# Performance work log

Measured on AMD Instinct MI355X. Metric: run time of the kernel, lower is better.

Reference implementation:

```python
import jax, jax.numpy as jnp
import numpy as np

B, N = 128, 2048
QUERY_DIM, NODE_DIM, OUT_DIM = 256, 128, 256
LAMBDA_INIT = 0.8
LN_EPS = 1e-5


def setup_inputs() -> dict:
    key = jax.random.key(0)
    ks = jax.random.split(key, 8)
    fp_vec = jax.random.normal(ks[0], (B, QUERY_DIM), dtype=jnp.float32)
    node_mat = jax.random.normal(ks[1], (B, N, NODE_DIM), dtype=jnp.float32)
    mask = jax.random.uniform(ks[2], (B, N)) < 0.75
    s = 1.0 / np.sqrt(QUERY_DIM)
    Wq1 = jax.random.uniform(ks[3], (NODE_DIM, QUERY_DIM), minval=-s, maxval=s, dtype=jnp.float32)
    Wq2 = jax.random.uniform(ks[4], (NODE_DIM, QUERY_DIM), minval=-s, maxval=s, dtype=jnp.float32)
    s2 = 1.0 / np.sqrt(NODE_DIM)
    Wk = jax.random.uniform(ks[5], (NODE_DIM, NODE_DIM), minval=-s2, maxval=s2, dtype=jnp.float32)
    Wv = jax.random.uniform(ks[6], (OUT_DIM, NODE_DIM), minval=-s2, maxval=s2, dtype=jnp.float32)
    lambda_logit = jnp.zeros((1,), dtype=jnp.float32)
    gamma = jnp.ones((OUT_DIM,), dtype=jnp.float32)
    beta = jnp.zeros((OUT_DIM,), dtype=jnp.float32)
    return {"fp_vec": fp_vec, "node_mat": node_mat, "mask": mask,
            "Wq1": Wq1, "Wq2": Wq2, "Wk": Wk, "Wv": Wv,
            "lambda_logit": lambda_logit, "gamma": gamma, "beta": beta}


def reference(fp_vec, node_mat, mask, Wq1, Wq2, Wk, Wv, lambda_logit, gamma, beta):
    node_dim = node_mat.shape[-1]
    inv_scale = 1.0 / jnp.sqrt(jnp.asarray(node_dim, jnp.float32))
    # projections (torch Linear: y = x @ W.T)
    q1 = fp_vec @ Wq1.T            # (B, node_dim)
    q2 = fp_vec @ Wq2.T            # (B, node_dim)
    k = jnp.einsum('bnd,ed->bne', node_mat, Wk)   # (B, N, node_dim)
    v = jnp.einsum('bnd,od->bno', node_mat, Wv)   # (B, N, out_dim)
    # single-query scores over nodes
    s1 = jnp.einsum('bd,bnd->bn', q1, k) * inv_scale
    s2 = jnp.einsum('bd,bnd->bn', q2, k) * inv_scale
    pad = jnp.where(mask, 0.0, -1e9).astype(s1.dtype)  # (B, N)
    A1 = jax.nn.softmax(s1 + pad, axis=-1)
    A2 = jax.nn.softmax(s2 + pad, axis=-1)
    lam = LAMBDA_INIT + jax.nn.sigmoid(lambda_logit) * 0.2  # (1,)
    A_diff = A1 - lam * A2         # dropout inactive (eval)
    z = jnp.einsum('bn,bno->bo', A_diff, v)  # (B, out_dim)
    # LayerNorm
    mu = jnp.mean(z, axis=-1, keepdims=True)
    var = jnp.mean(jnp.square(z - mu), axis=-1, keepdims=True)
    return (z - mu) * jax.lax.rsqrt(var + LN_EPS) * gamma + beta
```

## Files before the change

### kernel.cpp

```cpp
#include <hip/hip_runtime.h>
#include <hip/hip_bf16.h>
#include <math.h>

#define BB 128
#define NN 2048
#define ND 128
#define QD 256
#define OD 256
#define CHUNKS 16
#define ROWS_PER_CHUNK (NN / CHUNKS)
#define PART_STRIDE 260

#define EXP2F(x) __builtin_amdgcn_exp2f(x)

__global__ __launch_bounds__(128) void proj_kernel(
    const float* __restrict__ fp_vec, const float* __restrict__ Wq1,
    const float* __restrict__ Wq2, const float* __restrict__ Wk,
    float* __restrict__ qk1g, float* __restrict__ qk2g)
{
  __shared__ __align__(16) float fp_s[QD];
  __shared__ float q1_s[ND];
  __shared__ float q2_s[ND];
  const int b = blockIdx.x, t = threadIdx.x;
  fp_s[t]       = fp_vec[b * QD + t];
  fp_s[t + 128] = fp_vec[b * QD + 128 + t];
  __syncthreads();
  float a1 = 0.f, a2 = 0.f;
  const float4* w1p = (const float4*)(Wq1 + t * QD);
  const float4* w2p = (const float4*)(Wq2 + t * QD);
  #pragma unroll 8
  for (int q = 0; q < QD / 4; ++q) {
    float4 wa = w1p[q], wb = w2p[q];
    float4 f = *(const float4*)&fp_s[q * 4];
    a1 += f.x * wa.x + f.y * wa.y + f.z * wa.z + f.w * wa.w;
    a2 += f.x * wb.x + f.y * wb.y + f.z * wb.z + f.w * wb.w;
  }
  q1_s[t] = a1;
  q2_s[t] = a2;
  __syncthreads();
  float k1 = 0.f, k2 = 0.f;
  #pragma unroll 8
  for (int e = 0; e < ND; ++e) {
    float wv = Wk[e * ND + t];
    k1 += q1_s[e] * wv;
    k2 += q2_s[e] * wv;
  }
  const float cscale = 0.08838834764831845f * 1.4426950408889634f;
  qk1g[b * ND + t] = k1 * cscale;
  qk2g[b * ND + t] = k2 * cscale;
}

__global__ __launch_bounds__(256) void attn_kernel(
    const float* __restrict__ node, const int* __restrict__ mask,
    const float* __restrict__ qk1g, const float* __restrict__ qk2g,
    float* __restrict__ part)
{
  const int bid = blockIdx.x;
  const int b = bid >> 4;
  const int c = bid & (CHUNKS - 1);
  const int t = threadIdx.x;
  const int wave = t >> 6;
  const int lane = t & 63;
  const int half = lane >> 5;
  const int hl = lane & 31;

  __shared__ float pad_s[ROWS_PER_CHUNK];
  __shared__ float sl1[8], sl2[8];
  __shared__ __align__(16) float sw1[8][ND];
  __shared__ __align__(16) float sw2[8][ND];

  const int chunk_row0 = c * ROWS_PER_CHUNK;
  if (t < ROWS_PER_CHUNK)
    pad_s[t] = mask[b * NN + chunk_row0 + t] ? 0.f : -1e9f;
  __syncthreads();

  const float4 qk1 = *(const float4*)(qk1g + b * ND + hl * 4);
  const float4 qk2 = *(const float4*)(qk2g + b * ND + hl * 4);

  const int row_base = chunk_row0 + wave * 32;
  const float* nb = node + (size_t)b * NN * ND;

  float l1 = 0.f, l2 = 0.f;
  float4 w1 = make_float4(0.f, 0.f, 0.f, 0.f);
  float4 w2 = make_float4(0.f, 0.f, 0.f, 0.f);

  #pragma unroll 8
  for (int j = 0; j < 16; ++j) {
    const int rw = 2 * j + half;
    const float4 x = *(const float4*)(nb + (size_t)(row_base + rw) * ND + hl * 4);
    const float pad = pad_s[wave * 32 + rw];

    float d1 = x.x * qk1.x + x.y * qk1.y + x.z * qk1.z + x.w * qk1.w;
    float d2 = x.x * qk2.x + x.y * qk2.y + x.z * qk2.z + x.w * qk2.w;
    #pragma unroll
    for (int off = 1; off < 32; off <<= 1) {
      d1 += __shfl_xor(d1, off, 64);
      d2 += __shfl_xor(d2, off, 64);
    }
    const float p1 = EXP2F(d1 + pad);
    const float p2 = EXP2F(d2 + pad);
    l1 += p1;
    l2 += p2;
    w1.x += p1 * x.x; w1.y += p1 * x.y; w1.z += p1 * x.z; w1.w += p1 * x.w;
    w2.x += p2 * x.x; w2.y += p2 * x.y; w2.z += p2 * x.z; w2.w += p2 * x.w;
  }

  const int hidx = wave * 2 + half;
  if (hl == 0) { sl1[hidx] = l1; sl2[hidx] = l2; }
  *(float4*)&sw1[hidx][hl * 4] = w1;
  *(float4*)&sw2[hidx][hl * 4] = w2;
  __syncthreads();

  float* po = part + (size_t)bid * PART_STRIDE;
  if (t == 0) {
    float L1 = 0.f, L2 = 0.f;
    #pragma unroll
    for (int i = 0; i < 8; ++i) { L1 += sl1[i]; L2 += sl2[i]; }
    po[0] = L1; po[1] = L2;
  }
  if (t < ND) {
    float W1 = 0.f, W2 = 0.f;
    #pragma unroll
    for (int i = 0; i < 8; ++i) {
      W1 += sw1[i][t];
      W2 += sw2[i][t];
    }
    po[4 + t]   = W1;
    po[132 + t] = W2;
  }
}

__global__ __launch_bounds__(256) void finish_kernel(
    const float* __restrict__ part, const float* __restrict__ Wv,
    const float* __restrict__ lambda_logit, const float* __restrict__ gamma,
    const float* __restrict__ beta, float* __restrict__ out)
{
  const int b = blockIdx.x, t = threadIdx.x;
  __shared__ __align__(16) float wd_s[ND];
  __shared__ float red[8];

  const float lam = 0.8f + 0.2f / (1.f + __expf(-lambda_logit[0]));
  const float* pb = part + (size_t)b * CHUNKS * PART_STRIDE;

  if (t < ND) {
    float L1 = 0.f, L2 = 0.f, W1 = 0.f, W2 = 0.f;
    #pragma unroll
    for (int i = 0; i < CHUNKS; ++i) {
      const float* pc = pb + (size_t)i * PART_STRIDE;
      L1 += pc[0];
      L2 += pc[1];
      W1 += pc[4 + t];
      W2 += pc[132 + t];
    }
    wd_s[t] = W1 / L1 - lam * (W2 / L2);
  }
  __syncthreads();

  float z = 0.f;
  const float4* wvp = (const float4*)(Wv + t * ND);
  #pragma unroll 8
  for (int d = 0; d < ND / 4; ++d) {
    const float4 w = wvp[d];
    const float4 f = *(const float4*)&wd_s[d * 4];
    z += f.x * w.x + f.y * w.y + f.z * w.z + f.w * w.w;
  }

  const int wave = t >> 6, lane = t & 63;
  float s = z;
  #pragma unroll
  for (int off = 32; off; off >>= 1) s += __shfl_xor(s, off, 64);
  if (lane == 0) red[wave] = s;
  __syncthreads();
  const float mu = (red[0] + red[1] + red[2] + red[3]) * (1.f / OD);
  const float dz = z - mu;
  float vs = dz * dz;
  #pragma unroll
  for (int off = 32; off; off >>= 1) vs += __shfl_xor(vs, off, 64);
  if (lane == 0) red[wave + 4] = vs;
  __syncthreads();
  const float var = (red[4] + red[5] + red[6] + red[7]) * (1.f / OD);
  out[b * OD + t] = dz * rsqrtf(var + 1e-5f) * gamma[t] + beta[t];
}

extern "C" void kernel_launch(void* const* d_in, const int* in_sizes, int n_in,
                              void* d_out, int out_size, void* d_ws, size_t ws_size,
                              hipStream_t stream) {
  const float* fp_vec = (const float*)d_in[0];
  const float* node   = (const float*)d_in[1];
  const int*   mask   = (const int*)d_in[2];
  const float* Wq1    = (const float*)d_in[3];
  const float* Wq2    = (const float*)d_in[4];
  const float* Wk     = (const float*)d_in[5];
  const float* Wv     = (const float*)d_in[6];
  const float* ll     = (const float*)d_in[7];
  const float* gamma  = (const float*)d_in[8];
  const float* beta   = (const float*)d_in[9];
  float* out = (float*)d_out;

  float* qk1g = (float*)d_ws;
  float* qk2g = qk1g + BB * ND;
  float* part = qk2g + BB * ND;

  proj_kernel<<<BB, 128, 0, stream>>>(fp_vec, Wq1, Wq2, Wk, qk1g, qk2g);
  attn_kernel<<<BB * CHUNKS, 256, 0, stream>>>(node, mask, qk1g, qk2g, part);
  finish_kernel<<<BB, 256, 0, stream>>>(part, Wv, ll, gamma, beta, out);
}
```

Measured before the change: 239.6 us.

## Double-buffer node tiles through LDS with register prefetch in attention kernel

```diff
diff --git a/kernel.cpp b/kernel.cpp
--- a/kernel.cpp
+++ b/kernel.cpp
@@ -9,6 +9,8 @@
 #define OD 256
 #define CHUNKS 16
 #define ROWS_PER_CHUNK (NN / CHUNKS)
+#define TILE_ROWS 16
+#define TILES (ROWS_PER_CHUNK / TILE_ROWS)
 #define PART_STRIDE 260
 
 #define EXP2F(x) __builtin_amdgcn_exp2f(x)
@@ -64,69 +66,94 @@
   const int half = lane >> 5;
   const int hl = lane & 31;
 
+  __shared__ __align__(16) float tile_s[2][TILE_ROWS * ND];
   __shared__ float pad_s[ROWS_PER_CHUNK];
-  __shared__ float sl1[8], sl2[8];
-  __shared__ __align__(16) float sw1[8][ND];
-  __shared__ __align__(16) float sw2[8][ND];
+  __shared__ float sl1[4], sl2[4];
+  __shared__ __align__(16) float sw1[4][ND], sw2[4][ND];
 
   const int chunk_row0 = c * ROWS_PER_CHUNK;
   if (t < ROWS_PER_CHUNK)
     pad_s[t] = mask[b * NN + chunk_row0 + t] ? 0.f : -1e9f;
-  __syncthreads();
 
   const float4 qk1 = *(const float4*)(qk1g + b * ND + hl * 4);
   const float4 qk2 = *(const float4*)(qk2g + b * ND + hl * 4);
 
-  const int row_base = chunk_row0 + wave * 32;
-  const float* nb = node + (size_t)b * NN * ND;
+  const float4* gc = (const float4*)(node + (size_t)b * NN * ND
+                                     + (size_t)chunk_row0 * ND);
+
+  {
+    float4 a0 = gc[t];
+    float4 a1 = gc[t + 256];
+    float4* d = (float4*)tile_s[0];
+    d[t] = a0;
+    d[t + 256] = a1;
+  }
+  __syncthreads();
 
   float l1 = 0.f, l2 = 0.f;
   float4 w1 = make_float4(0.f, 0.f, 0.f, 0.f);
   float4 w2 = make_float4(0.f, 0.f, 0.f, 0.f);
 
-  #pragma unroll 8
-  for (int j = 0; j < 16; ++j) {
-    const int rw = 2 * j + half;
-    const float4 x = *(const float4*)(nb + (size_t)(row_base + rw) * ND + hl * 4);
-    const float pad = pad_s[wave * 32 + rw];
-
-    float d1 = x.x * qk1.x + x.y * qk1.y + x.z * qk1.z + x.w * qk1.w;
-    float d2 = x.x * qk2.x + x.y * qk2.y + x.z * qk2.z + x.w * qk2.w;
+  #pragma unroll
+  for (int tt = 0; tt < TILES; ++tt) {
+    float4 y0, y1;
+    if (tt + 1 < TILES) {
+      y0 = gc[(tt + 1) * (TILE_ROWS * ND / 4) + t];
+      y1 = gc[(tt + 1) * (TILE_ROWS * ND / 4) + t + 256];
+    }
+    __builtin_amdgcn_sched_barrier(0);
+
+    const float* buf = tile_s[tt & 1];
     #pragma unroll
-    for (int off = 1; off < 32; off <<= 1) {
-      d1 += __shfl_xor(d1, off, 64);
-      d2 += __shfl_xor(d2, off, 64);
-    }
-    const float p1 = EXP2F(d1 + pad);
-    const float p2 = EXP2F(d2 + pad);
-    l1 += p1;
-    l2 += p2;
-    w1.x += p1 * x.x; w1.y += p1 * x.y; w1.z += p1 * x.z; w1.w += p1 * x.w;
-    w2.x += p2 * x.x; w2.y += p2 * x.y; w2.z += p2 * x.z; w2.w += p2 * x.w;
-  }
-
-  const int hidx = wave * 2 + half;
-  if (hl == 0) { sl1[hidx] = l1; sl2[hidx] = l2; }
-  *(float4*)&sw1[hidx][hl * 4] = w1;
-  *(float4*)&sw2[hidx][hl * 4] = w2;
+    for (int i = 0; i < 2; ++i) {
+      const int r = 4 * wave + 2 * i + half;
+      const float4 x = *(const float4*)&buf[r * ND + hl * 4];
+      const float pad = pad_s[tt * TILE_ROWS + r];
+
+      float d1 = x.x * qk1.x + x.y * qk1.y + x.z * qk1.z + x.w * qk1.w;
+      float d2 = x.x * qk2.x + x.y * qk2.y + x.z * qk2.z + x.w * qk2.w;
+      #pragma unroll
+      for (int off = 1; off < 32; off <<= 1) {
+        d1 += __shfl_xor(d1, off, 64);
+        d2 += __shfl_xor(d2, off, 64);
+      }
+      const float p1 = EXP2F(d1 + pad);
+      const float p2 = EXP2F(d2 + pad);
+      l1 += p1;
+      l2 += p2;
+      w1.x += p1 * x.x; w1.y += p1 * x.y; w1.z += p1 * x.z; w1.w += p1 * x.w;
+      w2.x += p2 * x.x; w2.y += p2 * x.y; w2.z += p2 * x.z; w2.w += p2 * x.w;
+    }
+    __syncthreads();
+    if (tt + 1 < TILES) {
+      float4* d = (float4*)tile_s[(tt + 1) & 1];
+      d[t] = y0;
+      d[t + 256] = y1;
+    }
+    __syncthreads();
+  }
+
+  l1 += __shfl_xor(l1, 32, 64);
+  l2 += __shfl_xor(l2, 32, 64);
+  w1.x += __shfl_xor(w1.x, 32, 64); w1.y += __shfl_xor(w1.y, 32, 64);
+  w1.z += __shfl_xor(w1.z, 32, 64); w1.w += __shfl_xor(w1.w, 32, 64);
+  w2.x += __shfl_xor(w2.x, 32, 64); w2.y += __shfl_xor(w2.y, 32, 64);
+  w2.z += __shfl_xor(w2.z, 32, 64); w2.w += __shfl_xor(w2.w, 32, 64);
+  if (half == 0) {
+    *(float4*)&sw1[wave][hl * 4] = w1;
+    *(float4*)&sw2[wave][hl * 4] = w2;
+    if (hl == 0) { sl1[wave] = l1; sl2[wave] = l2; }
+  }
   __syncthreads();
 
   float* po = part + (size_t)bid * PART_STRIDE;
   if (t == 0) {
-    float L1 = 0.f, L2 = 0.f;
-    #pragma unroll
-    for (int i = 0; i < 8; ++i) { L1 += sl1[i]; L2 += sl2[i]; }
-    po[0] = L1; po[1] = L2;
+    po[0] = sl1[0] + sl1[1] + sl1[2] + sl1[3];
+    po[1] = sl2[0] + sl2[1] + sl2[2] + sl2[3];
   }
   if (t < ND) {
-    float W1 = 0.f, W2 = 0.f;
-    #pragma unroll
-    for (int i = 0; i < 8; ++i) {
-      W1 += sw1[i][t];
-      W2 += sw2[i][t];
-    }
-    po[4 + t]   = W1;
-    po[132 + t] = W2;
+    po[4 + t]   = sw1[0][t] + sw1[1][t] + sw1[2][t] + sw1[3][t];
+    po[132 + t] = sw2[0][t] + sw2[1][t] + sw2[2][t] + sw2[3][t];
   }
 }
 
```

After: 242.0 us. No clear change (+1.0%).
